# Kernel optimization log

Hardware: AMD Instinct MI355X
Metric: run time of the kernel (lower is better)

Reference implementation:

```python
import jax, jax.numpy as jnp
import numpy as np

B, S, DIN, DOUT = 4, 2048, 4096, 11008


def setup_inputs() -> dict:
    key = jax.random.key(0)
    k1, k2, k3, k4 = jax.random.split(key, 4)
    x = jax.random.normal(k1, (B, S, DIN), dtype=jnp.float32)
    # signed int8 quantized weights, stored as int32 for portability
    Wq = jax.random.randint(k2, (DOUT, DIN), -127, 128, dtype=jnp.int32)
    # per-output-channel scales (positive, clamped >= 1e-8 as in from_float)
    scale = jnp.maximum(jax.random.uniform(k3, (DOUT,), dtype=jnp.float32) * 0.02, 1e-8)
    b = jax.random.normal(k4, (DOUT,), dtype=jnp.float32)
    return {"x": x, "Wq": Wq, "scale": scale, "b": b}


def reference(x, Wq, scale, b):
    # dequantize: W[o, i] = Wq[o, i] * scale[o]
    W = Wq.astype(x.dtype) * scale[:, None].astype(x.dtype)
    # y = x @ W.T + bias  (leading dims flattened implicitly by einsum)
    y = jnp.einsum('bsi,oi->bso', x, W) + b.astype(x.dtype)
    # act_type == 'gelu' -> act_id = 1 (exact GELU, matching torch default)
    y = jax.nn.gelu(y, approximate=False)
    return y
```

## Files before the change

kernel.cpp:

```cpp
#include <hip/hip_runtime.h>
#include <cstdint>
#include <cstddef>


#define Msz 8192
#define Nsz 11008
#define Ksz 4096

#define TM 256
#define TN 256
#define TK 128
#define NT (Ksz / TK)
#define NI (NT / 2)
#define HALF (128 * TK)
#define NWG ((Msz / TM) * (Nsz / TN))
#define CPX (NWG / 8)

#define BM 128
#define BN 128

typedef __attribute__((ext_vector_type(4))) int int4v;
typedef __attribute__((ext_vector_type(8))) short short8;
typedef __attribute__((ext_vector_type(4))) float floatx4;

__device__ __forceinline__ void async16(const void* g, void* l) {
  __builtin_amdgcn_global_load_lds(
      (const __attribute__((address_space(1))) void*)g,
      (__attribute__((address_space(3))) void*)l, 16, 0, 0);
}

__global__ __launch_bounds__(256) void quant_x(
    const float* __restrict__ x, signed char* __restrict__ xq,
    float* __restrict__ qs) {
  const int row = blockIdx.x;
  const int tid = threadIdx.x;
  const int lane = tid & 63;
  const int wave = tid >> 6;
  const float4* xr = (const float4*)(x + (size_t)row * Ksz);

  float4 v[4];
  float m = 0.f;
#pragma unroll
  for (int t = 0; t < 4; ++t) {
    v[t] = xr[tid + t * 256];
    m = fmaxf(m, fmaxf(fmaxf(fabsf(v[t].x), fabsf(v[t].y)),
                       fmaxf(fabsf(v[t].z), fabsf(v[t].w))));
  }
#pragma unroll
  for (int o = 32; o > 0; o >>= 1) m = fmaxf(m, __shfl_down(m, o));
  __shared__ float sm[4];
  if (lane == 0) sm[wave] = m;
  __syncthreads();
  const float am = fmaxf(fmaxf(sm[0], sm[1]), fmaxf(sm[2], sm[3]));
  const float rs = am > 0.f ? 127.0f / am : 0.f;
  if (tid == 0) qs[row] = am * (1.0f / 127.0f);

  unsigned* outd = (unsigned*)(xq + (size_t)row * Ksz);
#pragma unroll
  for (int t = 0; t < 4; ++t) {
    int q0 = __float2int_rn(fminf(fmaxf(v[t].x * rs, -127.f), 127.f));
    int q1 = __float2int_rn(fminf(fmaxf(v[t].y * rs, -127.f), 127.f));
    int q2 = __float2int_rn(fminf(fmaxf(v[t].z * rs, -127.f), 127.f));
    int q3 = __float2int_rn(fminf(fmaxf(v[t].w * rs, -127.f), 127.f));
    outd[tid + t * 256] = (unsigned)(q0 & 255) | ((unsigned)(q1 & 255) << 8) |
                          ((unsigned)(q2 & 255) << 16) | ((unsigned)q3 << 24);
  }
}

__global__ __launch_bounds__(256) void pack_w(const int4* __restrict__ w,
                                              unsigned* __restrict__ o) {
  const unsigned gid = blockIdx.x * 256 + threadIdx.x;
  const unsigned stride = 11008u * 256u;
#pragma unroll
  for (int t = 0; t < 4; ++t) {
    const unsigned idx = gid + t * stride;
    const int4 a = w[idx];
    o[idx] = (unsigned)(a.x & 255) | ((unsigned)(a.y & 255) << 8) |
             ((unsigned)(a.z & 255) << 16) | ((unsigned)a.w << 24);
  }
}

__device__ __forceinline__ void stage_half(signed char* dst,
                                           const signed char* src, int grow0,
                                           int kt, int tid) {
  const int c = tid & 7;
  const int k0 = kt * TK;
#pragma unroll
  for (int rho = 0; rho < 2; ++rho) {
    const int rl = rho * 64 + (tid >> 3);
    async16(src + (size_t)(grow0 + rl) * Ksz + k0 + ((c ^ (rl & 7)) << 4),
            dst + rho * 8192 + tid * 16);
  }
}

__device__ __forceinline__ int4v ldfrag(const signed char* s, int row,
                                        int slot) {
  return *(const int4v*)(s + row * TK + (((slot) ^ (row & 7)) << 4));
}

#define PHASE(b, q, LOADB, SDST, GSRC, GROW0, KT, VM)                        \
  {                                                                          \
    int4v afr[2][2];                                                         \
    _Pragma("unroll") for (int ii = 0; ii < 2; ++ii) {                       \
      const int ar = wr * 128 + ((2 * (q) + ii) << 4) + (lane & 15);         \
      _Pragma("unroll") for (int kk = 0; kk < 2; ++kk)                       \
          afr[ii][kk] = ldfrag(sA[b], ar, kk * 4 + (lane >> 4));             \
    }                                                                        \
    if (LOADB) {                                                             \
      _Pragma("unroll") for (int jj = 0; jj < 4; ++jj) {                     \
        const int br = wc * 64 + (jj << 4) + (lane & 15);                    \
        _Pragma("unroll") for (int kk = 0; kk < 2; ++kk)                     \
            bfr[jj][kk] = ldfrag(sB[b], br, kk * 4 + (lane >> 4));           \
      }                                                                      \
    }                                                                        \
    stage_half(SDST, GSRC, GROW0, KT, tid);                                  \
    __builtin_amdgcn_sched_barrier(0);    \
    __builtin_amdgcn_s_barrier();                                            \
    __builtin_amdgcn_sched_barrier(0);     \
    __builtin_amdgcn_s_setprio(1);                                           \
    _Pragma("unroll") for (int kk = 0; kk < 2; ++kk)                         \
        _Pragma("unroll") for (int ii = 0; ii < 2; ++ii)                     \
            _Pragma("unroll") for (int jj = 0; jj < 4; ++jj)                 \
                acc[2 * (q) + ii][jj] =                                      \
                    __builtin_amdgcn_mfma_i32_16x16x64_i8(                   \
                        afr[ii][kk], bfr[jj][kk], acc[2 * (q) + ii][jj], 0,  \
                        0, 0);                                               \
    __builtin_amdgcn_s_setprio(0);                                           \
    __builtin_amdgcn_sched_barrier(0);                                       \
    if (VM) asm volatile("s_waitcnt vmcnt(4)" ::: "memory");                 \
    __builtin_amdgcn_s_barrier();                                            \
  }

__global__ __launch_bounds__(512, 2) void gemm_i8(
    const signed char* __restrict__ A8,
    const signed char* __restrict__ B8,
    const float* __restrict__ qs,
    const float* __restrict__ scale, const float* __restrict__ bias,
    float* __restrict__ out) {
  __shared__ signed char sA[2][TM * TK];
  __shared__ signed char sB[2][TN * TK];

  const int tid = threadIdx.x;
  const int wave = tid >> 6;
  const int lane = tid & 63;
  const int wr = wave >> 2;
  const int wc = wave & 3;

  const int bid = blockIdx.x;
  const int swz = (bid & 7) * CPX + (bid >> 3);
  const int bm0 = (swz & 31) * TM;
  const int bn0 = (swz >> 5) * TN;

  int4v acc[8][4];
#pragma unroll
  for (int i = 0; i < 8; ++i)
#pragma unroll
    for (int j = 0; j < 4; ++j) acc[i][j] = (int4v)0;
  int4v bfr[4][2];

  stage_half(sA[0], A8, bm0, 0, tid);
  stage_half(sA[0] + HALF, A8, bm0 + 128, 0, tid);
  stage_half(sB[0], B8, bn0, 0, tid);
  stage_half(sB[0] + HALF, B8, bn0 + 128, 0, tid);
  stage_half(sB[1], B8, bn0, 1, tid);
  stage_half(sB[1] + HALF, B8, bn0 + 128, 1, tid);
  asm volatile("s_waitcnt vmcnt(4)" ::: "memory");
  __builtin_amdgcn_s_barrier();

  for (int j = 0; j < NI; ++j) {
    const int tA1 = 2 * j + 1;
    const int tB2 = (2 * j + 2 < NT) ? 2 * j + 2 : NT - 1;
    const int tB3 = (2 * j + 3 < NT) ? 2 * j + 3 : NT - 1;
    PHASE(0, 0, true, sA[1], A8, bm0, tA1, false)
    PHASE(0, 1, false, sA[1] + HALF, A8, bm0 + 128, tA1, false)
    PHASE(0, 2, false, sB[0], B8, bn0, tB2, false)
    PHASE(0, 3, false, sB[0] + HALF, B8, bn0 + 128, tB2, true)
    PHASE(1, 0, true, sA[0], A8, bm0, tB2, false)
    PHASE(1, 1, false, sA[0] + HALF, A8, bm0 + 128, tB2, false)
    PHASE(1, 2, false, sB[1], B8, bn0, tB3, false)
    PHASE(1, 3, false, sB[1] + HALF, B8, bn0 + 128, tB3, true)
  }
  asm volatile("s_waitcnt vmcnt(0)" ::: "memory");

  float sc[4], bb[4];
#pragma unroll
  for (int jj = 0; jj < 4; ++jj) {
    const int col = bn0 + wc * 64 + jj * 16 + (lane & 15);
    sc[jj] = scale[col];
    bb[jj] = bias[col];
  }
#pragma unroll
  for (int i = 0; i < 8; ++i) {
    const int row0 = bm0 + wr * 128 + i * 16 + (lane >> 4) * 4;
    float qv[4];
#pragma unroll
    for (int r = 0; r < 4; ++r) qv[r] = qs[row0 + r];
#pragma unroll
    for (int jj = 0; jj < 4; ++jj) {
      const int col = bn0 + wc * 64 + jj * 16 + (lane & 15);
#pragma unroll
      for (int r = 0; r < 4; ++r) {
        float v = (float)acc[i][jj][r] * (qv[r] * sc[jj]) + bb[jj];
        v = 0.5f * v * (1.0f + erff(v * 0.7071067811865476f));
        out[(size_t)(row0 + r) * Nsz + col] = v;
      }
    }
  }
}

__device__ __forceinline__ unsigned int f2bf(float f) {
  unsigned int u = __builtin_bit_cast(unsigned int, f);
  unsigned int r = u + 0x7FFFu + ((u >> 16) & 1u);
  return r >> 16;
}

__global__ __launch_bounds__(256) void gemm_bf16_inline(
    const float* __restrict__ Af, const int* __restrict__ Bi,
    const float* __restrict__ scale, const float* __restrict__ bias,
    float* __restrict__ out) {
  __shared__ unsigned short sA[BM * 32];
  __shared__ unsigned short sB[BN * 32];
  const int tid = threadIdx.x;
  const int wave = tid >> 6;
  const int lane = tid & 63;
  const int bn0 = blockIdx.x * BN;
  const int bm0 = blockIdx.y * BM;
  const int mw = (wave >> 1) * 64;
  const int nw = (wave & 1) * 64;
  floatx4 acc[4][4];
#pragma unroll
  for (int i = 0; i < 4; ++i)
#pragma unroll
    for (int j = 0; j < 4; ++j) acc[i][j] = (floatx4)0.f;
  for (int k0 = 0; k0 < Ksz; k0 += 32) {
#pragma unroll
    for (int it = 0; it < 4; ++it) {
      const int f = tid + it * 256;
      const int row = f >> 3;
      const int c4 = (f & 7) * 4;
      const float4 v = *(const float4*)(Af + (size_t)(bm0 + row) * Ksz + k0 + c4);
      uint2 p;
      p.x = f2bf(v.x) | (f2bf(v.y) << 16);
      p.y = f2bf(v.z) | (f2bf(v.w) << 16);
      *(uint2*)&sA[row * 32 + c4] = p;
      const int4 w2 = *(const int4*)(Bi + (size_t)(bn0 + row) * Ksz + k0 + c4);
      uint2 q;
      q.x = f2bf((float)w2.x) | (f2bf((float)w2.y) << 16);
      q.y = f2bf((float)w2.z) | (f2bf((float)w2.w) << 16);
      *(uint2*)&sB[row * 32 + c4] = q;
    }
    __syncthreads();
    short8 af[4], bfr[4];
    const int kof2 = (lane >> 4) * 8;
#pragma unroll
    for (int i = 0; i < 4; ++i) {
      af[i] = *(const short8*)&sA[(mw + i * 16 + (lane & 15)) * 32 + kof2];
      bfr[i] = *(const short8*)&sB[(nw + i * 16 + (lane & 15)) * 32 + kof2];
    }
#pragma unroll
    for (int i = 0; i < 4; ++i)
#pragma unroll
      for (int j = 0; j < 4; ++j)
        acc[i][j] =
            __builtin_amdgcn_mfma_f32_16x16x32_bf16(af[i], bfr[j], acc[i][j], 0, 0, 0);
    __syncthreads();
  }
#pragma unroll
  for (int j = 0; j < 4; ++j) {
    const int col = bn0 + nw + j * 16 + (lane & 15);
    const float s = scale[col];
    const float bb = bias[col];
#pragma unroll
    for (int i = 0; i < 4; ++i) {
      const int row0 = bm0 + mw + i * 16 + (lane >> 4) * 4;
#pragma unroll
      for (int r = 0; r < 4; ++r) {
        float v = acc[i][j][r] * s + bb;
        v = 0.5f * v * (1.0f + erff(v * 0.7071067811865476f));
        out[(size_t)(row0 + r) * Nsz + col] = v;
      }
    }
  }
}

extern "C" void kernel_launch(void* const* d_in, const int* in_sizes, int n_in,
                              void* d_out, int out_size, void* d_ws, size_t ws_size,
                              hipStream_t stream) {
  const float* x = (const float*)d_in[0];
  const int* Wq = (const int*)d_in[1];
  const float* scale = (const float*)d_in[2];
  const float* bias = (const float*)d_in[3];
  float* out = (float*)d_out;

  const size_t nx = (size_t)Msz * Ksz;
  const size_t nwq = (size_t)Nsz * Ksz;
  const size_t need = nx + nwq + Msz * sizeof(float);

  if (ws_size >= need) {
    signed char* xq = (signed char*)d_ws;
    signed char* wp = xq + nx;
    float* qsd = (float*)(wp + nwq);
    quant_x<<<dim3(Msz), dim3(256), 0, stream>>>(x, xq, qsd);
    pack_w<<<dim3((unsigned)(nwq / (16 * 256))), dim3(256), 0, stream>>>(
        (const int4*)Wq, (unsigned*)wp);
    gemm_i8<<<dim3(NWG), dim3(512), 0, stream>>>(xq, wp, qsd, scale, bias, out);
  } else {
    dim3 grid(Nsz / BN, Msz / BM);
    gemm_bf16_inline<<<grid, dim3(256), 0, stream>>>(x, Wq, scale, bias, out);
  }
}
```

Measured before the change: 1.134 ms.

## Stage A tiles in quarter slices to prefetch a full tile ahead

Replaces the half-tile A staging with finer 32-row-per-half slices issued one per phase, so the next A tile is loaded across all eight phases instead of only the first two. B loads are interleaved in the middle phases, and vmcnt waits are retuned per phase. The goal is to spread global-to-LDS traffic evenly and keep more loads in flight, hiding memory latency behind the MFMA work. The hand-set vmcnt counts are fragile, and a miscounted wait could cause races or extra stalls.

Measured after the change: 1.084 ms. -4.5%, faster.

```diff
diff --git a/kernel.cpp b/kernel.cpp
--- a/kernel.cpp
+++ b/kernel.cpp
@@ -93,30 +93,43 @@
   }
 }
 
+__device__ __forceinline__ void stage_Aslice(signed char* dst,
+                                             const signed char* src, int grow0,
+                                             int kt, int q, int tid) {
+  const int half = tid >> 8;
+  const int s = (tid & 255) >> 3;
+  const int c = tid & 7;
+  const int row = half * 128 + q * 32 + s;
+  async16(src + (size_t)(grow0 + row) * Ksz + kt * TK + ((c ^ (s & 7)) << 4),
+          dst + half * 16384 + q * 4096 + (tid & 255) * 16);
+}
+
 __device__ __forceinline__ int4v ldfrag(const signed char* s, int row,
                                         int slot) {
   return *(const int4v*)(s + row * TK + (((slot) ^ (row & 7)) << 4));
 }
 
-#define PHASE(b, q, LOADB, SDST, GSRC, GROW0, KT, VM)                        \
+#define VMW(N) asm volatile("s_waitcnt vmcnt(" #N ")" ::: "memory")
+
+#define PHASE(pA, pB, q, LOADB, STAGE_CODE, WAIT_CODE)                       \
   {                                                                          \
     int4v afr[2][2];                                                         \
     _Pragma("unroll") for (int ii = 0; ii < 2; ++ii) {                       \
       const int ar = wr * 128 + ((2 * (q) + ii) << 4) + (lane & 15);         \
       _Pragma("unroll") for (int kk = 0; kk < 2; ++kk)                       \
-          afr[ii][kk] = ldfrag(sA[b], ar, kk * 4 + (lane >> 4));             \
+          afr[ii][kk] = ldfrag(pA, ar, kk * 4 + (lane >> 4));                \
     }                                                                        \
     if (LOADB) {                                                             \
       _Pragma("unroll") for (int jj = 0; jj < 4; ++jj) {                     \
         const int br = wc * 64 + (jj << 4) + (lane & 15);                    \
         _Pragma("unroll") for (int kk = 0; kk < 2; ++kk)                     \
-            bfr[jj][kk] = ldfrag(sB[b], br, kk * 4 + (lane >> 4));           \
+            bfr[jj][kk] = ldfrag(pB, br, kk * 4 + (lane >> 4));              \
       }                                                                      \
     }                                                                        \
-    stage_half(SDST, GSRC, GROW0, KT, tid);                                  \
-    __builtin_amdgcn_sched_barrier(0);    \
+    STAGE_CODE                                                               \
+    __builtin_amdgcn_sched_barrier(0);                                       \
     __builtin_amdgcn_s_barrier();                                            \
-    __builtin_amdgcn_sched_barrier(0);     \
+    __builtin_amdgcn_sched_barrier(0);                                       \
     __builtin_amdgcn_s_setprio(1);                                           \
     _Pragma("unroll") for (int kk = 0; kk < 2; ++kk)                         \
         _Pragma("unroll") for (int ii = 0; ii < 2; ++ii)                     \
@@ -127,7 +140,7 @@
                         0, 0);                                               \
     __builtin_amdgcn_s_setprio(0);                                           \
     __builtin_amdgcn_sched_barrier(0);                                       \
-    if (VM) asm volatile("s_waitcnt vmcnt(4)" ::: "memory");                 \
+    WAIT_CODE;                                                               \
     __builtin_amdgcn_s_barrier();                                            \
   }
 
@@ -137,8 +150,12 @@
     const float* __restrict__ qs,
     const float* __restrict__ scale, const float* __restrict__ bias,
     float* __restrict__ out) {
-  __shared__ signed char sA[2][TM * TK];
-  __shared__ signed char sB[2][TN * TK];
+  __shared__ signed char sAbuf[2][TM * TK];
+  __shared__ signed char sBbuf[2][TN * TK];
+  signed char* sA0 = sAbuf[0];
+  signed char* sA1 = sAbuf[1];
+  signed char* sB0 = sBbuf[0];
+  signed char* sB1 = sBbuf[1];
 
   const int tid = threadIdx.x;
   const int wave = tid >> 6;
@@ -158,27 +175,48 @@
     for (int j = 0; j < 4; ++j) acc[i][j] = (int4v)0;
   int4v bfr[4][2];
 
-  stage_half(sA[0], A8, bm0, 0, tid);
-  stage_half(sA[0] + HALF, A8, bm0 + 128, 0, tid);
-  stage_half(sB[0], B8, bn0, 0, tid);
-  stage_half(sB[0] + HALF, B8, bn0 + 128, 0, tid);
-  stage_half(sB[1], B8, bn0, 1, tid);
-  stage_half(sB[1] + HALF, B8, bn0 + 128, 1, tid);
-  asm volatile("s_waitcnt vmcnt(4)" ::: "memory");
+  stage_Aslice(sA0, A8, bm0, 0, 0, tid);
+  stage_half(sB0, B8, bn0, 0, tid);
+  stage_Aslice(sA0, A8, bm0, 0, 1, tid);
+  stage_half(sB0 + HALF, B8, bn0 + 128, 0, tid);
+  stage_Aslice(sA0, A8, bm0, 0, 2, tid);
+  stage_Aslice(sA0, A8, bm0, 0, 3, tid);
+  stage_Aslice(sA1, A8, bm0, 1, 0, tid);
+  stage_half(sB1, B8, bn0, 1, tid);
+  stage_Aslice(sA1, A8, bm0, 1, 1, tid);
+  stage_half(sB1 + HALF, B8, bn0 + 128, 1, tid);
+  stage_Aslice(sA1, A8, bm0, 1, 2, tid);
+  VMW(9);
   __builtin_amdgcn_s_barrier();
 
   for (int j = 0; j < NI; ++j) {
-    const int tA1 = 2 * j + 1;
-    const int tB2 = (2 * j + 2 < NT) ? 2 * j + 2 : NT - 1;
-    const int tB3 = (2 * j + 3 < NT) ? 2 * j + 3 : NT - 1;
-    PHASE(0, 0, true, sA[1], A8, bm0, tA1, false)
-    PHASE(0, 1, false, sA[1] + HALF, A8, bm0 + 128, tA1, false)
-    PHASE(0, 2, false, sB[0], B8, bn0, tB2, false)
-    PHASE(0, 3, false, sB[0] + HALF, B8, bn0 + 128, tB2, true)
-    PHASE(1, 0, true, sA[0], A8, bm0, tB2, false)
-    PHASE(1, 1, false, sA[0] + HALF, A8, bm0 + 128, tB2, false)
-    PHASE(1, 2, false, sB[1], B8, bn0, tB3, false)
-    PHASE(1, 3, false, sB[1] + HALF, B8, bn0 + 128, tB3, true)
+    const int t1 = 2 * j + 1;
+    const int t2 = (2 * j + 2 < NT) ? 2 * j + 2 : NT - 1;
+    const int t3 = (2 * j + 3 < NT) ? 2 * j + 3 : NT - 1;
+    PHASE(sA0, sB0, 0, true,
+          { stage_Aslice(sA1, A8, bm0, t1, 3, tid); }, {})
+    PHASE(sA0, sB0, 1, false,
+          { stage_Aslice(sA0, A8, bm0, t2, 0, tid);
+            stage_half(sB0, B8, bn0, t2, tid); },
+          VMW(12))
+    PHASE(sA0, sB0, 2, false,
+          { stage_Aslice(sA0, A8, bm0, t2, 1, tid);
+            stage_half(sB0 + HALF, B8, bn0 + 128, t2, tid); },
+          VMW(14))
+    PHASE(sA0, sB0, 3, false,
+          { stage_Aslice(sA0, A8, bm0, t2, 2, tid); }, VMW(9))
+    PHASE(sA1, sB1, 0, true,
+          { stage_Aslice(sA0, A8, bm0, t2, 3, tid); }, VMW(12))
+    PHASE(sA1, sB1, 1, false,
+          { stage_Aslice(sA1, A8, bm0, t3, 0, tid);
+            stage_half(sB1, B8, bn0, t3, tid); },
+          VMW(12))
+    PHASE(sA1, sB1, 2, false,
+          { stage_Aslice(sA1, A8, bm0, t3, 1, tid);
+            stage_half(sB1 + HALF, B8, bn0 + 128, t3, tid); },
+          VMW(14))
+    PHASE(sA1, sB1, 3, false,
+          { stage_Aslice(sA1, A8, bm0, t3, 2, tid); }, VMW(9))
   }
   asm volatile("s_waitcnt vmcnt(0)" ::: "memory");
 
```
